# Optimization experiments

Measured on AMD Instinct MI355X. Metric: run time of the kernel, lower is better.

## Reference

```python
import math
import jax, jax.numpy as jnp
import numpy as np

N_HEAD = 16
N_GROUPS = 32
EPS = 1e-05


def gelu(x):
    return 0.5 * x * (1.0 + jnp.tanh(math.sqrt(2.0 / math.pi) * (x + 0.044715 * x ** 3)))


def dp_group_norm(x, weight, bias, num_groups=N_GROUPS, eps=EPS):
    # x: [B, T, H]. torch F.group_norm on transposed [B, H, T] normalizes over
    # (channels_per_group, T) jointly per (batch, group).
    B, T, H = x.shape
    xg = x.reshape(B, T, num_groups, H // num_groups)
    mean = jnp.mean(xg, axis=(1, 3), keepdims=True)
    var = jnp.mean((xg - mean) ** 2, axis=(1, 3), keepdims=True)
    xn = ((xg - mean) / jnp.sqrt(var + eps)).reshape(B, T, H)
    return xn * weight + bias


def attention(x, w_attn, b_attn, w_aproj, b_aproj):
    B, T, H = x.shape
    hd = H // N_HEAD
    qkv = x @ w_attn + b_attn                      # [B, T, 3H]
    q, k, v = jnp.split(qkv, 3, axis=-1)
    q = q.reshape(B, T, N_HEAD, hd).transpose(0, 2, 1, 3)   # [B, nh, T, hd]
    k = k.reshape(B, T, N_HEAD, hd).transpose(0, 2, 1, 3)   # [B, nh, T, hd]
    v = v.reshape(B, T, N_HEAD, hd).transpose(0, 2, 1, 3)
    w = jnp.einsum('bhqd,bhkd->bhqk', q, k)        # no 1/sqrt(d): scale=False
    causal = jnp.tril(jnp.ones((T, T), dtype=x.dtype))
    w = w * causal - 1e10 * (1.0 - causal)
    w = jax.nn.softmax(w, axis=-1)
    a = jnp.einsum('bhqk,bhkd->bhqd', w, v)        # [B, nh, T, hd]
    a = a.transpose(0, 2, 1, 3).reshape(B, T, H)
    a = a @ w_aproj + b_aproj
    present = jnp.stack((k, v))                    # [2, B, nh, T, hd]
    return a, present


def setup_inputs() -> dict:
    key = jax.random.key(0)
    ks = jax.random.split(key, 6)
    B, T, H = 2, 2048, 1024
    return {
        'x': jax.random.normal(ks[0], (B, T, H), dtype=jnp.float32),
        'w_attn': jax.random.normal(ks[1], (H, 3 * H), dtype=jnp.float32) * 0.02,
        'b_attn': jnp.zeros((3 * H,), dtype=jnp.float32),
        'w_aproj': jax.random.normal(ks[2], (H, H), dtype=jnp.float32) * 0.02,
        'b_aproj': jnp.zeros((H,), dtype=jnp.float32),
        'ln1_w': jnp.ones((H,), dtype=jnp.float32),
        'ln1_b': jnp.zeros((H,), dtype=jnp.float32),
        'ln2_w': jnp.ones((H,), dtype=jnp.float32),
        'ln2_b': jnp.zeros((H,), dtype=jnp.float32),
        'w_fc': jax.random.normal(ks[3], (H, 4 * H), dtype=jnp.float32) * 0.02,
        'b_fc': jnp.zeros((4 * H,), dtype=jnp.float32),
        'w_mproj': jax.random.normal(ks[4], (4 * H, H), dtype=jnp.float32) * 0.02,
        'b_mproj': jnp.zeros((H,), dtype=jnp.float32),
    }


def reference(x, w_attn, b_attn, w_aproj, b_aproj, ln1_w, ln1_b, ln2_w, ln2_b,
              w_fc, b_fc, w_mproj, b_mproj):
    a, present = attention(dp_group_norm(x, ln1_w, ln1_b), w_attn, b_attn, w_aproj, b_aproj)
    x = x + a
    h = gelu(dp_group_norm(x, ln2_w, ln2_b) @ w_fc + b_fc)
    m = h @ w_mproj + b_mproj
    x = x + m
    return (x, present)
```

## Files before the change

kernel.cpp:

```cpp
#include <hip/hip_runtime.h>

#define B_  2
#define T_  2048
#define H_  1024
#define NH_ 16
#define HD_ 64
#define M_  (B_*T_)
#define PS_ 72

typedef __bf16 bf16x8 __attribute__((ext_vector_type(8)));
typedef float  floatx4 __attribute__((ext_vector_type(4)));

typedef __attribute__((address_space(1))) const unsigned int gas_u32;
typedef __attribute__((address_space(3))) unsigned int       las_u32;

__device__ __forceinline__ void gload_lds16(const __bf16* g, __bf16* l) {
    __builtin_amdgcn_global_load_lds((gas_u32*)g, (las_u32*)l, 16, 0, 0);
}

__global__ __launch_bounds__(256) void transpose_bf16(
    const float* __restrict__ in, __bf16* __restrict__ out, int K, int N)
{
    __shared__ float tile[32][33];
    const int k0 = blockIdx.x * 32, n0 = blockIdx.y * 32;
    const int tx = threadIdx.x & 31, ty = threadIdx.x >> 5;
#pragma unroll
    for (int i = 0; i < 32; i += 8)
        tile[ty + i][tx] = in[(size_t)(k0 + ty + i) * N + (n0 + tx)];
    __syncthreads();
#pragma unroll
    for (int i = 0; i < 32; i += 8)
        out[(size_t)(n0 + ty + i) * K + (k0 + tx)] = (__bf16)tile[tx][ty + i];
}

__global__ __launch_bounds__(256) void transpose_v(
    const __bf16* __restrict__ vb, __bf16* __restrict__ vtb)
{
    __shared__ __bf16 tile[32][33];
    const int bh = blockIdx.x;
    const int t0 = blockIdx.y * 32, d0 = blockIdx.z * 32;
    const __bf16* src = vb  + (size_t)bh * T_ * HD_;
    __bf16*       dst = vtb + (size_t)bh * HD_ * T_;
    const int tx = threadIdx.x & 31, ty = threadIdx.x >> 5;
#pragma unroll
    for (int i = 0; i < 32; i += 8)
        tile[ty + i][tx] = src[(size_t)(t0 + ty + i) * HD_ + (d0 + tx)];
    __syncthreads();
#pragma unroll
    for (int i = 0; i < 32; i += 8)
        dst[(size_t)(d0 + ty + i) * T_ + (t0 + tx)] = tile[tx][ty + i];
}

__global__ __launch_bounds__(256) void gn_partial(
    const float* __restrict__ x, float2* __restrict__ part)
{
    const int bg = blockIdx.x, chunk = blockIdx.y;
    const int batch = bg >> 5, g = bg & 31;
    const float* xp = x + (size_t)batch * T_ * H_ + g * 32;
    float s = 0.f, ss = 0.f;
    for (int i = threadIdx.x; i < 128 * 32; i += 256) {
        const int t = chunk * 128 + (i >> 5), c = i & 31;
        const float v = xp[(size_t)t * H_ + c];
        s += v; ss += v * v;
    }
#pragma unroll
    for (int off = 32; off > 0; off >>= 1) {
        s  += __shfl_down(s,  off, 64);
        ss += __shfl_down(ss, off, 64);
    }
    __shared__ float rs[4], rss[4];
    const int wv = threadIdx.x >> 6, lane = threadIdx.x & 63;
    if (lane == 0) { rs[wv] = s; rss[wv] = ss; }
    __syncthreads();
    if (threadIdx.x == 0)
        part[bg * 16 + chunk] =
            make_float2(rs[0] + rs[1] + rs[2] + rs[3],
                        rss[0] + rss[1] + rss[2] + rss[3]);
}

__global__ __launch_bounds__(64) void gn_finalize(
    const float2* __restrict__ part, float2* __restrict__ stats)
{
    const int bg = threadIdx.x;
    float s = 0.f, ss = 0.f;
#pragma unroll
    for (int i = 0; i < 16; ++i) {
        const float2 p = part[bg * 16 + i];
        s += p.x; ss += p.y;
    }
    const float inv = 1.f / (float)(T_ * 32);
    const float mean = s * inv;
    const float var  = ss * inv - mean * mean;
    stats[bg] = make_float2(mean, rsqrtf(var + 1e-5f));
}

__global__ __launch_bounds__(256) void gn_apply(
    const float* __restrict__ x, const float2* __restrict__ stats,
    const float* __restrict__ w, const float* __restrict__ bsc,
    __bf16* __restrict__ out)
{
    const size_t idx = ((size_t)blockIdx.x * 256 + threadIdx.x) * 4;
    const int h = (int)(idx & (H_ - 1));
    const int batch = (int)(idx >> 21);
    const float2 mr = stats[batch * 32 + (h >> 5)];
    const float4 xv = *(const float4*)(x + idx);
    const float4 wv = *(const float4*)(w + h);
    const float4 bv = *(const float4*)(bsc + h);
    __bf16 o[4];
    o[0] = (__bf16)((xv.x - mr.x) * mr.y * wv.x + bv.x);
    o[1] = (__bf16)((xv.y - mr.x) * mr.y * wv.y + bv.y);
    o[2] = (__bf16)((xv.z - mr.x) * mr.y * wv.z + bv.z);
    o[3] = (__bf16)((xv.w - mr.x) * mr.y * wv.w + bv.w);
    *(uint2*)(out + idx) = *(uint2*)o;
}

__device__ __forceinline__ void gemm_core256(
    const __bf16* __restrict__ A, const __bf16* __restrict__ BT,
    int K, int m0, int n0, __bf16* Sb, floatx4 (&acc)[8][4])
{
    const int tid = threadIdx.x, lane = tid & 63, wid = tid >> 6;
    const int quad = lane >> 4, l16 = lane & 15;
    const int wm = (wid >> 2) * 128, wn = (wid & 3) * 64;
    const int r0 = tid >> 2, cbs = tid & 3;
    const int sc  = ((cbs ^ ((r0 >> 1) & 3)) * 8);
    const int xq8 = (quad ^ ((l16 >> 1) & 3)) * 8;

    const __bf16* Ag = A  + (size_t)(m0 + r0) * K + sc;
    const __bf16* Bg = BT + (size_t)(n0 + r0) * K + sc;

#define STG256(b, kt)  do {                                                   \
    gload_lds16(Ag + (kt),                  Sb + (b)*16384 + tid*8);          \
    gload_lds16(Ag + (size_t)128*K + (kt),  Sb + (b)*16384 + 4096 + tid*8);   \
    gload_lds16(Bg + (kt),                  Sb + (b)*16384 + 8192 + tid*8);   \
    gload_lds16(Bg + (size_t)128*K + (kt),  Sb + (b)*16384 + 12288 + tid*8); } while (0)

    const int NT = K >> 5;
    STG256(0, 0);
    STG256(1, 32);
    STG256(2, 64);
    int cur = 0;
    for (int j = 0; j < NT; ++j) {
        const int kt = j << 5;
        if (j + 3 < NT) {
            STG256((cur + 3) & 3, kt + 96);
            asm volatile("s_waitcnt vmcnt(12)" ::: "memory");
        } else if (j + 2 < NT) {
            asm volatile("s_waitcnt vmcnt(8)" ::: "memory");
        } else if (j + 1 < NT) {
            asm volatile("s_waitcnt vmcnt(4)" ::: "memory");
        } else {
            asm volatile("s_waitcnt vmcnt(0)" ::: "memory");
        }
        __builtin_amdgcn_s_barrier();
        __builtin_amdgcn_sched_barrier(0);
        const __bf16* Ab = Sb + cur * 16384;
        const __bf16* Bb = Sb + cur * 16384 + 8192;
        bf16x8 af[8], bfg[4];
#pragma unroll
        for (int i = 0; i < 8; ++i)
            af[i]  = *(const bf16x8*)(Ab + (wm + i * 16 + l16) * 32 + xq8);
#pragma unroll
        for (int i = 0; i < 4; ++i)
            bfg[i] = *(const bf16x8*)(Bb + (wn + i * 16 + l16) * 32 + xq8);
        __builtin_amdgcn_s_setprio(1);
#pragma unroll
        for (int mi = 0; mi < 8; ++mi)
#pragma unroll
            for (int ni = 0; ni < 4; ++ni)
                acc[mi][ni] = __builtin_amdgcn_mfma_f32_16x16x32_bf16(
                    af[mi], bfg[ni], acc[mi][ni], 0, 0, 0);
        __builtin_amdgcn_s_setprio(0);
        __builtin_amdgcn_sched_barrier(0);
        __builtin_amdgcn_s_barrier();
        __builtin_amdgcn_sched_barrier(0);
        cur = (cur + 1) & 3;
    }
#undef STG256
}

#define GEMM256_PROLOGUE(KVAL)                                          \
    __shared__ __align__(16) __bf16 Sb[4 * 16384];          \
    const int m0 = blockIdx.x * 256, n0 = blockIdx.y * 256;             \
    floatx4 acc[8][4];                                                  \
    { floatx4 z = {0.f, 0.f, 0.f, 0.f};                                 \
      for (int i = 0; i < 8; ++i) for (int j = 0; j < 4; ++j) acc[i][j] = z; } \
    gemm_core256(A, BT, (KVAL), m0, n0, Sb, acc);                       \
    const int tid = threadIdx.x, lane = tid & 63, wid = tid >> 6;       \
    const int quad = lane >> 4, l16 = lane & 15;                        \
    const int wm = (wid >> 2) * 128, wn = (wid & 3) * 64;               \
    (void)tid;

__global__ __launch_bounds__(512) void gemm_qkv(
    const __bf16* __restrict__ A, const __bf16* __restrict__ BT,
    const float* __restrict__ bias, __bf16* __restrict__ qb,
    __bf16* __restrict__ kb, __bf16* __restrict__ vb,
    float* __restrict__ present)
{
    GEMM256_PROLOGUE(H_)
#pragma unroll
    for (int ni = 0; ni < 4; ++ni) {
        const int col = n0 + wn + ni * 16 + l16;
        const float bv = bias[col];
        const int which = col >> 10, c = col & 1023, hh = c >> 6, d = c & 63;
#pragma unroll
        for (int mi = 0; mi < 8; ++mi)
#pragma unroll
            for (int r = 0; r < 4; ++r) {
                const int row = m0 + wm + mi * 16 + quad * 4 + r;
                const int bb = row >> 11, t = row & 2047;
                const float v = acc[mi][ni][r] + bv;
                const size_t idx = (((size_t)bb * NH_ + hh) * T_ + t) * HD_ + d;
                if (which == 0)      qb[idx] = (__bf16)(v * 1.4426950408889634f);
                else if (which == 1) { kb[idx] = (__bf16)v; present[idx] = v; }
                else { vb[idx] = (__bf16)v;
                       present[(size_t)B_ * NH_ * T_ * HD_ + idx] = v; }
            }
    }
}

__global__ __launch_bounds__(512) void gemm_gelu(
    const __bf16* __restrict__ A, const __bf16* __restrict__ BT,
    const float* __restrict__ bias, __bf16* __restrict__ out)
{
    GEMM256_PROLOGUE(H_)
#pragma unroll
    for (int ni = 0; ni < 4; ++ni) {
        const int col = n0 + wn + ni * 16 + l16;
        const float bv = bias[col];
#pragma unroll
        for (int mi = 0; mi < 8; ++mi)
#pragma unroll
            for (int r = 0; r < 4; ++r) {
                const int row = m0 + wm + mi * 16 + quad * 4 + r;
                const float v = acc[mi][ni][r] + bv;
                const float e = exp2f(-2.3022082f * (v + 0.044715f * v * v * v));
                float rcp;
                asm("v_rcp_f32 %0, %1" : "=v"(rcp) : "v"(1.f + e));
                out[(size_t)row * (4 * H_) + col] = (__bf16)(v * rcp);
            }
    }
}

__global__ __launch_bounds__(256) void gemm_resid_n64(
    const __bf16* __restrict__ A, const __bf16* __restrict__ BT,
    const float* __restrict__ bias, const float* __restrict__ resid,
    float* __restrict__ out, int K, int N)
{
    __shared__ __align__(16) __bf16 As[3 * 8192], Bs[3 * 4096];
    const int m0 = blockIdx.x * 128, n0 = blockIdx.y * 64;
    const int tid  = threadIdx.x;
    const int lane = tid & 63, wv = tid >> 6;
    const int quad = lane >> 4, l16 = lane & 15;
    const int wm = (wv >> 1) * 64, wn = (wv & 1) * 32;
    const int r0 = tid >> 2;
    const int scs = (((tid & 3) ^ ((r0 >> 1) & 3)) * 8);
    const int xq8 = (quad ^ ((l16 >> 1) & 3)) * 8;

    floatx4 acc[4][2];
    { floatx4 z = {0.f, 0.f, 0.f, 0.f};
#pragma unroll
      for (int i = 0; i < 4; ++i) { acc[i][0] = z; acc[i][1] = z; } }

    const __bf16* Ag = A  + (size_t)(m0 + r0) * K + scs;
    const __bf16* Bg = BT + (size_t)(n0 + r0) * K + scs;

#define STGR(b, kt)  do {                                                     \
    _Pragma("unroll")                                                         \
    for (int s = 0; s < 2; ++s) {                                             \
        gload_lds16(Ag + (kt) + s * 32,                  As + (b)*8192 + s*4096 + tid*8);        \
        gload_lds16(Ag + (size_t)64 * K + (kt) + s * 32, As + (b)*8192 + s*4096 + 2048 + tid*8); \
        gload_lds16(Bg + (kt) + s * 32,                  Bs + (b)*4096 + s*2048 + tid*8);        \
    } } while (0)

    const int NT = K >> 6;
    STGR(0, 0);
    STGR(1, 64);
    int cur = 0;
    for (int j = 0; j < NT; ++j) {
        const int kt = j << 6;
        if (j + 2 < NT) {
            int nb = cur + 2; if (nb >= 3) nb -= 3;
            STGR(nb, kt + 128);
            asm volatile("s_waitcnt vmcnt(12)" ::: "memory");
        } else if (j + 1 < NT) {
            asm volatile("s_waitcnt vmcnt(6)" ::: "memory");
        } else {
            asm volatile("s_waitcnt vmcnt(0)" ::: "memory");
        }
        __builtin_amdgcn_s_barrier();
        __builtin_amdgcn_sched_barrier(0);
        const __bf16* Ab = As + cur * 8192;
        const __bf16* Bb = Bs + cur * 4096;
#pragma unroll
        for (int kk = 0; kk < 2; ++kk) {
            bf16x8 af[4], bfg[2];
#pragma unroll
            for (int i = 0; i < 4; ++i)
                af[i]  = *(const bf16x8*)(Ab + kk * 4096 + (wm + i * 16 + l16) * 32 + xq8);
#pragma unroll
            for (int i = 0; i < 2; ++i)
                bfg[i] = *(const bf16x8*)(Bb + kk * 2048 + (wn + i * 16 + l16) * 32 + xq8);
#pragma unroll
            for (int mi = 0; mi < 4; ++mi)
#pragma unroll
                for (int ni = 0; ni < 2; ++ni)
                    acc[mi][ni] = __builtin_amdgcn_mfma_f32_16x16x32_bf16(
                        af[mi], bfg[ni], acc[mi][ni], 0, 0, 0);
        }
        __builtin_amdgcn_sched_barrier(0);
        __builtin_amdgcn_s_barrier();
        __builtin_amdgcn_sched_barrier(0);
        cur = cur + 1; if (cur >= 3) cur = 0;
    }
#undef STGR

#pragma unroll
    for (int ni = 0; ni < 2; ++ni) {
        const int col = n0 + wn + ni * 16 + l16;
        const float bv = bias[col];
#pragma unroll
        for (int mi = 0; mi < 4; ++mi)
#pragma unroll
            for (int r = 0; r < 4; ++r) {
                const int row = m0 + wm + mi * 16 + quad * 4 + r;
                const size_t idx = (size_t)row * N + col;
                out[idx] = acc[mi][ni][r] + bv + resid[idx];
            }
    }
}

__global__ __launch_bounds__(256) void attn_kernel(
    const __bf16* __restrict__ qb, const __bf16* __restrict__ kb,
    const __bf16* __restrict__ vtb, __bf16* __restrict__ aout)
{
    const int bh = blockIdx.x;
    const int sp = 31 - blockIdx.y;
    const int bb = bh >> 4, hh = bh & 15;
    const __bf16* Q  = qb  + (size_t)bh * T_ * HD_;
    const __bf16* Kp = kb  + (size_t)bh * T_ * HD_;
    const __bf16* VT = vtb + (size_t)bh * HD_ * T_;
    __shared__ __align__(16) __bf16 Qs[2 * 2048];
    __shared__ __align__(16) __bf16 Ks[2][2 * 2048];
    __shared__ __align__(16) __bf16 Vs[2][2 * 2048];
    __shared__ __align__(16) __bf16 Ps[64 * PS_];

    const int tid = threadIdx.x, lane = tid & 63, wv = tid >> 6;
    const int quad = lane >> 4, l16 = lane & 15;
    const int sr = tid >> 2;
    const int scs = (((tid & 3) ^ ((sr >> 1) & 3)) * 8);
    const int xq8 = (quad ^ ((l16 >> 1) & 3)) * 8;

    const int q0 = sp * 64, nkt = sp + 1;

#pragma unroll
    for (int s = 0; s < 2; ++s) {
        gload_lds16(Q  + (size_t)(q0 + sr) * HD_ + s * 32 + scs, Qs + s * 2048 + tid * 8);
        gload_lds16(Kp + (size_t)sr * HD_ + s * 32 + scs, &Ks[0][s * 2048 + tid * 8]);
        gload_lds16(VT + (size_t)sr * T_  + s * 32 + scs, &Vs[0][s * 2048 + tid * 8]);
    }
    asm volatile("s_waitcnt vmcnt(0)" ::: "memory");
    __builtin_amdgcn_s_barrier();
    __builtin_amdgcn_sched_barrier(0);

    bf16x8 aq[2];
#pragma unroll
    for (int kk = 0; kk < 2; ++kk)
        aq[kk] = *(const bf16x8*)(Qs + kk * 2048 + (wv * 16 + l16) * 32 + xq8);

    float m_i[4], l_p[4];
    floatx4 Ov[4];
    { floatx4 z = {0.f, 0.f, 0.f, 0.f};
#pragma unroll
      for (int i = 0; i < 4; ++i) { Ov[i] = z; m_i[i] = -1e30f; l_p[i] = 0.f; } }

    int cur = 0;
    for (int kt = 0; kt < nkt; ++kt) {
        if (kt + 1 < nkt) {
            const int kn = (kt + 1) * 64;
#pragma unroll
            for (int s = 0; s < 2; ++s) {
                gload_lds16(Kp + (size_t)(kn + sr) * HD_ + s * 32 + scs,
                            &Ks[cur ^ 1][s * 2048 + tid * 8]);
                gload_lds16(VT + (size_t)sr * T_ + kn + s * 32 + scs,
                            &Vs[cur ^ 1][s * 2048 + tid * 8]);
            }
            asm volatile("s_waitcnt vmcnt(4)" ::: "memory");
        } else {
            asm volatile("s_waitcnt vmcnt(0)" ::: "memory");
        }
        __builtin_amdgcn_s_barrier();
        __builtin_amdgcn_sched_barrier(0);

        const __bf16* Kc = Ks[cur];
        const __bf16* Vc = Vs[cur];

        floatx4 sacc[4];
        { floatx4 z = {0.f, 0.f, 0.f, 0.f};
#pragma unroll
          for (int i = 0; i < 4; ++i) sacc[i] = z; }
#pragma unroll
        for (int kk = 0; kk < 2; ++kk)
#pragma unroll
            for (int ni = 0; ni < 4; ++ni) {
                const bf16x8 bk = *(const bf16x8*)(Kc + kk * 2048 + (ni * 16 + l16) * 32 + xq8);
                sacc[ni] = __builtin_amdgcn_mfma_f32_16x16x32_bf16(aq[kk], bk, sacc[ni], 0, 0, 0);
            }
        if (kt == sp) {
#pragma unroll
            for (int ni = 0; ni < 4; ++ni) {
                const int keyL = ni * 16 + l16;
#pragma unroll
                for (int r = 0; r < 4; ++r)
                    if (keyL > quad * 4 + r + wv * 16) sacc[ni][r] = -1e30f;
            }
        }
        float rml[4];
#pragma unroll
        for (int r = 0; r < 4; ++r)
            rml[r] = fmaxf(fmaxf(sacc[0][r], sacc[1][r]),
                           fmaxf(sacc[2][r], sacc[3][r]));
        float need = rml[0] - m_i[0];
#pragma unroll
        for (int r = 1; r < 4; ++r) need = fmaxf(need, rml[r] - m_i[r]);
        if (__any(need > 8.f)) {
#pragma unroll
            for (int off = 1; off < 16; off <<= 1)
#pragma unroll
                for (int r = 0; r < 4; ++r)
                    rml[r] = fmaxf(rml[r], __shfl_xor(rml[r], off, 64));
#pragma unroll
            for (int r = 0; r < 4; ++r) {
                const float mn = fmaxf(m_i[r], rml[r]);
                const float al = exp2f(m_i[r] - mn);
                m_i[r] = mn;
                l_p[r] *= al;
#pragma unroll
                for (int ni = 0; ni < 4; ++ni) Ov[ni][r] *= al;
            }
        }
#pragma unroll
        for (int ni = 0; ni < 4; ++ni)
#pragma unroll
            for (int r = 0; r < 4; ++r) {
                const float pe = exp2f(sacc[ni][r] - m_i[r]);
                sacc[ni][r] = pe;
                l_p[r] += pe;
            }
#pragma unroll
        for (int ni = 0; ni < 4; ++ni)
#pragma unroll
            for (int r = 0; r < 4; ++r)
                Ps[(wv * 16 + quad * 4 + r) * PS_ + ni * 16 + l16] = (__bf16)sacc[ni][r];
#pragma unroll
        for (int kk = 0; kk < 2; ++kk) {
            const bf16x8 ap = *(const bf16x8*)(Ps + (wv * 16 + l16) * PS_ + kk * 32 + quad * 8);
#pragma unroll
            for (int ni = 0; ni < 4; ++ni) {
                const bf16x8 bv2 = *(const bf16x8*)(Vc + kk * 2048 + (ni * 16 + l16) * 32 + xq8);
                Ov[ni] = __builtin_amdgcn_mfma_f32_16x16x32_bf16(ap, bv2, Ov[ni], 0, 0, 0);
            }
        }
        __builtin_amdgcn_sched_barrier(0);
        __builtin_amdgcn_s_barrier();
        __builtin_amdgcn_sched_barrier(0);
        cur ^= 1;
    }
#pragma unroll
    for (int off = 1; off < 16; off <<= 1)
#pragma unroll
        for (int r = 0; r < 4; ++r)
            l_p[r] += __shfl_xor(l_p[r], off, 64);
#pragma unroll
    for (int ni = 0; ni < 4; ++ni)
#pragma unroll
        for (int r = 0; r < 4; ++r) {
            const int t = q0 + wv * 16 + quad * 4 + r;
            aout[((size_t)(bb * T_ + t)) * H_ + hh * HD_ + ni * 16 + l16] =
                (__bf16)(Ov[ni][r] / l_p[r]);
        }
}

extern "C" void kernel_launch(void* const* d_in, const int* in_sizes, int n_in,
                              void* d_out, int out_size, void* d_ws, size_t ws_size,
                              hipStream_t stream)
{
    (void)in_sizes; (void)n_in; (void)out_size; (void)ws_size;
    const float* x       = (const float*)d_in[0];
    const float* w_attn  = (const float*)d_in[1];
    const float* b_attn  = (const float*)d_in[2];
    const float* w_aproj = (const float*)d_in[3];
    const float* b_aproj = (const float*)d_in[4];
    const float* ln1_w   = (const float*)d_in[5];
    const float* ln1_b   = (const float*)d_in[6];
    const float* ln2_w   = (const float*)d_in[7];
    const float* ln2_b   = (const float*)d_in[8];
    const float* w_fc    = (const float*)d_in[9];
    const float* b_fc    = (const float*)d_in[10];
    const float* w_mproj = (const float*)d_in[11];
    const float* b_mproj = (const float*)d_in[12];
    float* out = (float*)d_out;
    float* present = out + (size_t)M_ * H_;

    char* wp = (char*)d_ws;
    auto alloc = [&](size_t bytes) {
        void* p = (void*)wp; wp += (bytes + 255) & ~(size_t)255; return p;
    };
    __bf16* A1       = (__bf16*)alloc((size_t)M_ * H_ * 2);
    __bf16* A2       = (__bf16*)alloc((size_t)M_ * H_ * 2);
    __bf16* WattnT   = (__bf16*)alloc((size_t)3 * H_ * H_ * 2);
    __bf16* WaprojT  = (__bf16*)alloc((size_t)H_ * H_ * 2);
    __bf16* WfcT     = (__bf16*)alloc((size_t)4 * H_ * H_ * 2);
    __bf16* WmprojT  = (__bf16*)alloc((size_t)4 * H_ * H_ * 2);
    __bf16* qb       = (__bf16*)alloc((size_t)M_ * H_ * 2);
    __bf16* kb       = (__bf16*)alloc((size_t)M_ * H_ * 2);
    __bf16* vb       = (__bf16*)alloc((size_t)M_ * H_ * 2);
    __bf16* vtb      = (__bf16*)alloc((size_t)M_ * H_ * 2);
    __bf16* attn_out = (__bf16*)alloc((size_t)M_ * H_ * 2);
    float*  x2       = (float*) alloc((size_t)M_ * H_ * 4);
    __bf16* Hbuf     = (__bf16*)alloc((size_t)M_ * 4 * H_ * 2);
    float2* gn_part  = (float2*)alloc(64 * 16 * sizeof(float2));
    float2* gn_stats = (float2*)alloc(64 * sizeof(float2));

    transpose_bf16<<<dim3(H_/32, 3*H_/32), 256, 0, stream>>>(w_attn,  WattnT,  H_,   3*H_);
    transpose_bf16<<<dim3(H_/32, H_/32),   256, 0, stream>>>(w_aproj, WaprojT, H_,   H_);
    transpose_bf16<<<dim3(H_/32, 4*H_/32), 256, 0, stream>>>(w_fc,    WfcT,    H_,   4*H_);
    transpose_bf16<<<dim3(4*H_/32, H_/32), 256, 0, stream>>>(w_mproj, WmprojT, 4*H_, H_);

    gn_partial <<<dim3(64, 16), 256, 0, stream>>>(x, gn_part);
    gn_finalize<<<1, 64, 0, stream>>>(gn_part, gn_stats);
    gn_apply   <<<M_*H_/1024, 256, 0, stream>>>(x, gn_stats, ln1_w, ln1_b, A1);

    gemm_qkv<<<dim3(M_/256, 3*H_/256), 512, 0, stream>>>(A1, WattnT, b_attn,
                                                         qb, kb, vb, present);
    transpose_v<<<dim3(B_*NH_, T_/32, HD_/32), 256, 0, stream>>>(vb, vtb);
    attn_kernel<<<dim3(32, 32), 256, 0, stream>>>(qb, kb, vtb, attn_out);
    gemm_resid_n64<<<dim3(M_/128, H_/64), 256, 0, stream>>>(attn_out, WaprojT, b_aproj,
                                                            x, x2, H_, H_);

    gn_partial <<<dim3(64, 16), 256, 0, stream>>>(x2, gn_part);
    gn_finalize<<<1, 64, 0, stream>>>(gn_part, gn_stats);
    gn_apply   <<<M_*H_/1024, 256, 0, stream>>>(x2, gn_stats, ln2_w, ln2_b, A2);

    gemm_gelu<<<dim3(M_/256, 4*H_/256), 512, 0, stream>>>(A2, WfcT, b_fc, Hbuf);
    gemm_resid_n64<<<dim3(M_/128, H_/64), 256, 0, stream>>>(Hbuf, WmprojT, b_mproj,
                                                            x2, out, 4*H_, H_);
}
```

Before: 400.9 us.

## Fuse group-norm stats into GEMM epilogue and finalize inside gn_apply

Removes the gn_finalize kernel by having each gn_apply block reduce the 16 partial sums for its batch into shared memory. The second group-norm's partial statistics are now produced in the attention-projection GEMM epilogue, which drops a separate full read of x2 and one kernel launch. Separately, the attention kernel raises wave priority around its MFMA sections with s_setprio. In exchange, every gn_apply block redoes a small reduction, and the GEMM epilogue gains a shuffle reduction and a barrier.

```diff
diff --git a/kernel.cpp b/kernel.cpp
--- a/kernel.cpp
+++ b/kernel.cpp
@@ -78,31 +78,27 @@
                         rss[0] + rss[1] + rss[2] + rss[3]);
 }
 
-__global__ __launch_bounds__(64) void gn_finalize(
-    const float2* __restrict__ part, float2* __restrict__ stats)
-{
-    const int bg = threadIdx.x;
-    float s = 0.f, ss = 0.f;
-#pragma unroll
-    for (int i = 0; i < 16; ++i) {
-        const float2 p = part[bg * 16 + i];
-        s += p.x; ss += p.y;
-    }
-    const float inv = 1.f / (float)(T_ * 32);
-    const float mean = s * inv;
-    const float var  = ss * inv - mean * mean;
-    stats[bg] = make_float2(mean, rsqrtf(var + 1e-5f));
-}
-
 __global__ __launch_bounds__(256) void gn_apply(
-    const float* __restrict__ x, const float2* __restrict__ stats,
+    const float* __restrict__ x, const float2* __restrict__ part,
     const float* __restrict__ w, const float* __restrict__ bsc,
     __bf16* __restrict__ out)
 {
-    const size_t idx = ((size_t)blockIdx.x * 256 + threadIdx.x) * 4;
+    __shared__ float2 st[32];
+    const size_t base = (size_t)blockIdx.x * 1024;
+    const int batch = (int)(base >> 21);
+    if (threadIdx.x < 32) {
+        const float2* p = part + ((size_t)batch * 32 + threadIdx.x) * 16;
+        float s = 0.f, ss = 0.f;
+#pragma unroll
+        for (int i = 0; i < 16; ++i) { s += p[i].x; ss += p[i].y; }
+        const float inv = 1.f / (float)(T_ * 32);
+        const float mean = s * inv;
+        st[threadIdx.x] = make_float2(mean, rsqrtf(ss * inv - mean * mean + 1e-5f));
+    }
+    __syncthreads();
+    const size_t idx = base + (size_t)threadIdx.x * 4;
     const int h = (int)(idx & (H_ - 1));
-    const int batch = (int)(idx >> 21);
-    const float2 mr = stats[batch * 32 + (h >> 5)];
+    const float2 mr = st[h >> 5];
     const float4 xv = *(const float4*)(x + idx);
     const float4 wv = *(const float4*)(w + h);
     const float4 bv = *(const float4*)(bsc + h);
@@ -244,7 +240,7 @@
 __global__ __launch_bounds__(256) void gemm_resid_n64(
     const __bf16* __restrict__ A, const __bf16* __restrict__ BT,
     const float* __restrict__ bias, const float* __restrict__ resid,
-    float* __restrict__ out, int K, int N)
+    float* __restrict__ out, float2* __restrict__ gnp, int K, int N)
 {
     __shared__ __align__(16) __bf16 As[3 * 8192], Bs[3 * 4096];
     const int m0 = blockIdx.x * 128, n0 = blockIdx.y * 64;
@@ -314,6 +310,7 @@
     }
 #undef STGR
 
+    float s = 0.f, ss = 0.f;
 #pragma unroll
     for (int ni = 0; ni < 2; ++ni) {
         const int col = n0 + wn + ni * 16 + l16;
@@ -324,8 +321,28 @@
             for (int r = 0; r < 4; ++r) {
                 const int row = m0 + wm + mi * 16 + quad * 4 + r;
                 const size_t idx = (size_t)row * N + col;
-                out[idx] = acc[mi][ni][r] + bv + resid[idx];
-            }
+                const float v = acc[mi][ni][r] + bv + resid[idx];
+                out[idx] = v;
+                s += v; ss += v * v;
+            }
+    }
+    if (gnp) {
+        __shared__ float pr[4][2];
+#pragma unroll
+        for (int off = 32; off > 0; off >>= 1) {
+            s  += __shfl_down(s,  off, 64);
+            ss += __shfl_down(ss, off, 64);
+        }
+        if (lane == 0) { pr[wv][0] = s; pr[wv][1] = ss; }
+        __syncthreads();
+        if (tid < 2) {
+            const float S  = pr[tid][0] + pr[tid + 2][0];
+            const float SS = pr[tid][1] + pr[tid + 2][1];
+            const int batch = m0 >> 11;
+            const int mblk  = (m0 >> 7) & 15;
+            const int g     = (n0 >> 5) + tid;
+            gnp[((size_t)batch * 32 + g) * 16 + mblk] = make_float2(S, SS);
+        }
     }
 }
 
@@ -398,6 +415,7 @@
         { floatx4 z = {0.f, 0.f, 0.f, 0.f};
 #pragma unroll
           for (int i = 0; i < 4; ++i) sacc[i] = z; }
+        __builtin_amdgcn_s_setprio(1);
 #pragma unroll
         for (int kk = 0; kk < 2; ++kk)
 #pragma unroll
@@ -405,6 +423,7 @@
                 const bf16x8 bk = *(const bf16x8*)(Kc + kk * 2048 + (ni * 16 + l16) * 32 + xq8);
                 sacc[ni] = __builtin_amdgcn_mfma_f32_16x16x32_bf16(aq[kk], bk, sacc[ni], 0, 0, 0);
             }
+        __builtin_amdgcn_s_setprio(0);
         if (kt == sp) {
 #pragma unroll
             for (int ni = 0; ni < 4; ++ni) {
@@ -451,6 +470,7 @@
 #pragma unroll
             for (int r = 0; r < 4; ++r)
                 Ps[(wv * 16 + quad * 4 + r) * PS_ + ni * 16 + l16] = (__bf16)sacc[ni][r];
+        __builtin_amdgcn_s_setprio(1);
 #pragma unroll
         for (int kk = 0; kk < 2; ++kk) {
             const bf16x8 ap = *(const bf16x8*)(Ps + (wv * 16 + l16) * PS_ + kk * 32 + quad * 8);
@@ -460,6 +480,7 @@
                 Ov[ni] = __builtin_amdgcn_mfma_f32_16x16x32_bf16(ap, bv2, Ov[ni], 0, 0, 0);
             }
         }
+        __builtin_amdgcn_s_setprio(0);
         __builtin_amdgcn_sched_barrier(0);
         __builtin_amdgcn_s_barrier();
         __builtin_amdgcn_sched_barrier(0);
@@ -519,29 +540,25 @@
     float*  x2       = (float*) alloc((size_t)M_ * H_ * 4);
     __bf16* Hbuf     = (__bf16*)alloc((size_t)M_ * 4 * H_ * 2);
     float2* gn_part  = (float2*)alloc(64 * 16 * sizeof(float2));
-    float2* gn_stats = (float2*)alloc(64 * sizeof(float2));
 
     transpose_bf16<<<dim3(H_/32, 3*H_/32), 256, 0, stream>>>(w_attn,  WattnT,  H_,   3*H_);
     transpose_bf16<<<dim3(H_/32, H_/32),   256, 0, stream>>>(w_aproj, WaprojT, H_,   H_);
     transpose_bf16<<<dim3(H_/32, 4*H_/32), 256, 0, stream>>>(w_fc,    WfcT,    H_,   4*H_);
     transpose_bf16<<<dim3(4*H_/32, H_/32), 256, 0, stream>>>(w_mproj, WmprojT, 4*H_, H_);
 
-    gn_partial <<<dim3(64, 16), 256, 0, stream>>>(x, gn_part);
-    gn_finalize<<<1, 64, 0, stream>>>(gn_part, gn_stats);
-    gn_apply   <<<M_*H_/1024, 256, 0, stream>>>(x, gn_stats, ln1_w, ln1_b, A1);
+    gn_partial<<<dim3(64, 16), 256, 0, stream>>>(x, gn_part);
+    gn_apply  <<<M_*H_/1024, 256, 0, stream>>>(x, gn_part, ln1_w, ln1_b, A1);
 
     gemm_qkv<<<dim3(M_/256, 3*H_/256), 512, 0, stream>>>(A1, WattnT, b_attn,
                                                          qb, kb, vb, present);
     transpose_v<<<dim3(B_*NH_, T_/32, HD_/32), 256, 0, stream>>>(vb, vtb);
     attn_kernel<<<dim3(32, 32), 256, 0, stream>>>(qb, kb, vtb, attn_out);
     gemm_resid_n64<<<dim3(M_/128, H_/64), 256, 0, stream>>>(attn_out, WaprojT, b_aproj,
-                                                            x, x2, H_, H_);
-
-    gn_partial <<<dim3(64, 16), 256, 0, stream>>>(x2, gn_part);
-    gn_finalize<<<1, 64, 0, stream>>>(gn_part, gn_stats);
-    gn_apply   <<<M_*H_/1024, 256, 0, stream>>>(x2, gn_stats, ln2_w, ln2_b, A2);
+                                                            x, x2, gn_part, H_, H_);
+
+    gn_apply<<<M_*H_/1024, 256, 0, stream>>>(x2, gn_part, ln2_w, ln2_b, A2);
 
     gemm_gelu<<<dim3(M_/256, 4*H_/256), 512, 0, stream>>>(A2, WfcT, b_fc, Hbuf);
     gemm_resid_n64<<<dim3(M_/128, H_/64), 256, 0, stream>>>(Hbuf, WmprojT, b_mproj,
-                                                            x2, out, 4*H_, H_);
-}
+                                                            x2, out, nullptr, 4*H_, H_);
+}
```

Measured after the change: 390.8 us. 1.03x faster.
